# Performance work log

Hardware: AMD Instinct MI355X
Metric: run time of the kernel (lower is better)

## Reference

```python
import jax, jax.numpy as jnp
import numpy as np

NUM_USERS, NUM_ITEMS, NUM_GROUPS = 100000, 50000, 20000
D = 64
B, M = 16384, 50


def setup_inputs() -> dict:
    key = jax.random.key(0)
    ks = jax.random.split(key, 16)
    inp = {
        "group_inputs": jax.random.randint(ks[0], (B,), 0, NUM_GROUPS),
        "item_inputs": jax.random.randint(ks[1], (B,), 0, NUM_ITEMS),
        "member_ids": jax.random.randint(ks[2], (B, M), 0, NUM_USERS),
        "member_lengths": jax.random.randint(ks[3], (B,), 0, M),
        # embedding tables (xavier-ish scale)
        "user_table": jax.random.normal(ks[4], (NUM_USERS, D), jnp.float32) * 0.05,
        "item_table": jax.random.normal(ks[5], (NUM_ITEMS, D), jnp.float32) * 0.05,
        "group_table": jax.random.normal(ks[6], (NUM_GROUPS, D), jnp.float32) * 0.05,
        # attention MLP: 2D -> 16 -> 1
        "att_w1": jax.random.normal(ks[7], (2 * D, 16), jnp.float32) * 0.1,
        "att_b1": jnp.zeros((16,), jnp.float32),
        "att_w2": jax.random.normal(ks[8], (16, 1), jnp.float32) * 0.1,
        "att_b2": jnp.zeros((1,), jnp.float32),
        # predict MLP: 3D -> 8 -> 1
        "pred_w1": jax.random.normal(ks[9], (3 * D, 8), jnp.float32) * 0.1,
        "pred_b1": jnp.zeros((8,), jnp.float32),
        "pred_w2": jax.random.normal(ks[10], (8, 1), jnp.float32) * 0.1,
        "pred_b2": jnp.zeros((1,), jnp.float32),
    }
    return inp


def reference(group_inputs, item_inputs, member_ids, member_lengths,
              user_table, item_table, group_table,
              att_w1, att_b1, att_w2, att_b2,
              pred_w1, pred_b1, pred_w2, pred_b2):
    # mask: at least one valid member per group
    mask = jnp.arange(M)[None, :] <= member_lengths[:, None]          # [B, M] bool
    mem_e = user_table[member_ids]                                    # [B, M, D]
    item_e = item_table[item_inputs]                                  # [B, D]

    # attention over members: concat(member, item) -> 16 -> 1
    gi = jnp.concatenate(
        [mem_e, jnp.broadcast_to(item_e[:, None, :], mem_e.shape)], axis=-1)  # [B, M, 2D]
    h = jax.nn.relu(jnp.einsum('bmk,kh->bmh', gi, att_w1) + att_b1)   # [B, M, 16]
    scores = (jnp.einsum('bmh,ho->bmo', h, att_w2) + att_b2)[..., 0]  # [B, M]
    scores = jnp.where(mask, scores, -jnp.inf)
    at_wt = jax.nn.softmax(scores, axis=-1)                           # [B, M]

    g_att = jnp.einsum('bm,bmd->bd', at_wt, mem_e)                    # [B, D]
    g = g_att + group_table[group_inputs]                             # [B, D]

    elem = g * item_e
    new_e = jnp.concatenate([elem, g, item_e], axis=-1)               # [B, 3D]
    ph = jax.nn.relu(new_e @ pred_w1 + pred_b1)                       # [B, 8]
    y = jax.nn.sigmoid(ph @ pred_w2 + pred_b2)                        # [B, 1]
    return y
```

## Files before the change

kernel.cpp:

```cpp
#include <hip/hip_runtime.h>
#include <math.h>

constexpr int MM = 50;
constexpr int DD = 64;
constexpr int HH = 16;
constexpr int PH = 8;
constexpr int WAVES_PER_BLOCK = 4;

__global__ __launch_bounds__(256) void agree_kernel(
    const int* __restrict__ group_inputs,
    const int* __restrict__ item_inputs,
    const int* __restrict__ member_ids,
    const int* __restrict__ member_lengths,
    const float* __restrict__ user_table,
    const float* __restrict__ item_table,
    const float* __restrict__ group_table,
    const float* __restrict__ att_w1,
    const float* __restrict__ att_b1,
    const float* __restrict__ att_w2,
    const float* __restrict__ att_b2,
    const float* __restrict__ pred_w1,
    const float* __restrict__ pred_b1,
    const float* __restrict__ pred_w2,
    const float* __restrict__ pred_b2,
    float* __restrict__ out,
    int B)
{
    __shared__ float lds_wt[WAVES_PER_BLOCK][MM];
    __shared__ int   lds_id[WAVES_PER_BLOCK][MM];

    const int lane = threadIdx.x & 63;
    const int wave = threadIdx.x >> 6;
    const int b = blockIdx.x * WAVES_PER_BLOCK + wave;
    if (b >= B) return;

    const int my_m = (lane < MM) ? lane : (MM - 1);
    const int my_id = member_ids[b * MM + my_m];
    if (lane < MM) lds_id[wave][lane] = my_id;

    const int item_idx = item_inputs[b];
    const float item_d = item_table[(size_t)item_idx * DD + lane];

    float h[HH];
    {
        const float* w1row = att_w1 + (size_t)(DD + lane) * HH;
        #pragma unroll
        for (int j = 0; j < HH; ++j) h[j] = item_d * w1row[j];
        #pragma unroll
        for (int off = 32; off > 0; off >>= 1) {
            #pragma unroll
            for (int j = 0; j < HH; ++j) h[j] += __shfl_xor(h[j], off, 64);
        }
        #pragma unroll
        for (int j = 0; j < HH; ++j) h[j] += att_b1[j];
    }

    const float* myrow = user_table + (size_t)my_id * DD;
    #pragma unroll 4
    for (int d4 = 0; d4 < DD / 4; ++d4) {
        const float4 x = ((const float4*)myrow)[d4];
        const float* w1d = att_w1 + (size_t)(d4 * 4) * HH;
        #pragma unroll
        for (int j = 0; j < HH; ++j) {
            h[j] = fmaf(x.x, w1d[0 * HH + j], h[j]);
            h[j] = fmaf(x.y, w1d[1 * HH + j], h[j]);
            h[j] = fmaf(x.z, w1d[2 * HH + j], h[j]);
            h[j] = fmaf(x.w, w1d[3 * HH + j], h[j]);
        }
    }

    float score = att_b2[0];
    #pragma unroll
    for (int j = 0; j < HH; ++j) score = fmaf(fmaxf(h[j], 0.0f), att_w2[j], score);

    const int len = member_lengths[b];
    const bool valid = (lane < MM) && (lane <= len);
    score = valid ? score : -INFINITY;

    float mx = score;
    #pragma unroll
    for (int off = 32; off > 0; off >>= 1) mx = fmaxf(mx, __shfl_xor(mx, off, 64));
    float e = valid ? __expf(score - mx) : 0.0f;
    float sum = e;
    #pragma unroll
    for (int off = 32; off > 0; off >>= 1) sum += __shfl_xor(sum, off, 64);
    if (lane < MM) lds_wt[wave][lane] = e / sum;
    __builtin_amdgcn_s_waitcnt(0);

    const int mcnt = (len < MM - 1 ? len : MM - 1) + 1;
    float g = 0.0f;
    #pragma unroll 2
    for (int m = 0; m < mcnt; ++m) {
        const float wm  = lds_wt[wave][m];
        const int   idm = lds_id[wave][m];
        g = fmaf(wm, user_table[(size_t)idm * DD + lane], g);
    }
    const int gid = group_inputs[b];
    g += group_table[(size_t)gid * DD + lane];

    const float elem = g * item_d;
    float p[PH];
    {
        const float* pa = pred_w1 + (size_t)lane * PH;
        const float* pb = pred_w1 + (size_t)(DD + lane) * PH;
        const float* pc = pred_w1 + (size_t)(2 * DD + lane) * PH;
        #pragma unroll
        for (int j = 0; j < PH; ++j)
            p[j] = fmaf(elem, pa[j], fmaf(g, pb[j], item_d * pc[j]));
    }
    #pragma unroll
    for (int off = 32; off > 0; off >>= 1) {
        #pragma unroll
        for (int j = 0; j < PH; ++j) p[j] += __shfl_xor(p[j], off, 64);
    }

    if (lane == 0) {
        float acc = pred_b2[0];
        #pragma unroll
        for (int j = 0; j < PH; ++j)
            acc = fmaf(fmaxf(p[j] + pred_b1[j], 0.0f), pred_w2[j], acc);
        out[b] = 1.0f / (1.0f + __expf(-acc));
    }
}

extern "C" void kernel_launch(void* const* d_in, const int* in_sizes, int n_in,
                              void* d_out, int out_size, void* d_ws, size_t ws_size,
                              hipStream_t stream) {
    const int*   group_inputs   = (const int*)d_in[0];
    const int*   item_inputs    = (const int*)d_in[1];
    const int*   member_ids     = (const int*)d_in[2];
    const int*   member_lengths = (const int*)d_in[3];
    const float* user_table     = (const float*)d_in[4];
    const float* item_table     = (const float*)d_in[5];
    const float* group_table    = (const float*)d_in[6];
    const float* att_w1         = (const float*)d_in[7];
    const float* att_b1         = (const float*)d_in[8];
    const float* att_w2         = (const float*)d_in[9];
    const float* att_b2         = (const float*)d_in[10];
    const float* pred_w1        = (const float*)d_in[11];
    const float* pred_b1        = (const float*)d_in[12];
    const float* pred_w2        = (const float*)d_in[13];
    const float* pred_b2        = (const float*)d_in[14];
    float* out = (float*)d_out;

    const int B = in_sizes[0];
    const int blocks = (B + WAVES_PER_BLOCK - 1) / WAVES_PER_BLOCK;
    agree_kernel<<<blocks, 256, 0, stream>>>(
        group_inputs, item_inputs, member_ids, member_lengths,
        user_table, item_table, group_table,
        att_w1, att_b1, att_w2, att_b2,
        pred_w1, pred_b1, pred_w2, pred_b2,
        out, B);
}
```

Measured before the change: 158.9 us.

## Precompute per-row attention projections for user and item tables before main kernel

Adds a precompute kernel that multiplies every user and item embedding row by its half of the attention first-layer weights once per call, writing 16-float projections to workspace. The main kernel then gets each member's hidden activations by loading 16 floats and adding the item projection, instead of doing a 64x16 matvec per member. The weighted-sum gather is also unrolled by four with weight and id packed together in LDS. The trade-off is that all 150k table rows get projected even though only about 820k member lookups are needed, costing a full read of both tables plus an extra launch.

After: 144.5 us. -9.1%, faster.

```diff
diff --git a/kernel.cpp b/kernel.cpp
--- a/kernel.cpp
+++ b/kernel.cpp
@@ -7,7 +7,159 @@
 constexpr int PH = 8;
 constexpr int WAVES_PER_BLOCK = 4;
 
-__global__ __launch_bounds__(256) void agree_kernel(
+__global__ __launch_bounds__(256) void precompute_kernel(
+    const float* __restrict__ user_table,
+    const float* __restrict__ item_table,
+    const float* __restrict__ att_w1,
+    const float* __restrict__ att_b1,
+    float* __restrict__ U,
+    float* __restrict__ I,
+    int nU, int nI, int userBlocks)
+{
+    const bool isU = (int)blockIdx.x < userBlocks;
+    const int row = isU ? ((int)blockIdx.x * 256 + (int)threadIdx.x)
+                        : (((int)blockIdx.x - userBlocks) * 256 + (int)threadIdx.x);
+    const int n = isU ? nU : nI;
+    if (row >= n) return;
+
+    const float* __restrict__ src = isU ? user_table : item_table;
+    const float* __restrict__ w1  = isU ? att_w1 : (att_w1 + DD * HH);
+    const float4* rp = (const float4*)(src + (size_t)row * DD);
+
+    float acc[HH];
+    #pragma unroll
+    for (int j = 0; j < HH; ++j) acc[j] = isU ? 0.0f : att_b1[j];
+
+    #pragma unroll 4
+    for (int d4 = 0; d4 < DD / 4; ++d4) {
+        const float4 x = rp[d4];
+        const float* w = w1 + (size_t)(d4 * 4) * HH;
+        #pragma unroll
+        for (int j = 0; j < HH; ++j) {
+            acc[j] = fmaf(x.x, w[0 * HH + j], acc[j]);
+            acc[j] = fmaf(x.y, w[1 * HH + j], acc[j]);
+            acc[j] = fmaf(x.z, w[2 * HH + j], acc[j]);
+            acc[j] = fmaf(x.w, w[3 * HH + j], acc[j]);
+        }
+    }
+
+    float4* o4 = (float4*)((isU ? U : I) + (size_t)row * HH);
+    o4[0] = make_float4(acc[0],  acc[1],  acc[2],  acc[3]);
+    o4[1] = make_float4(acc[4],  acc[5],  acc[6],  acc[7]);
+    o4[2] = make_float4(acc[8],  acc[9],  acc[10], acc[11]);
+    o4[3] = make_float4(acc[12], acc[13], acc[14], acc[15]);
+}
+
+__global__ __launch_bounds__(256) void agree_main(
+    const int* __restrict__ group_inputs,
+    const int* __restrict__ item_inputs,
+    const int* __restrict__ member_ids,
+    const int* __restrict__ member_lengths,
+    const float* __restrict__ user_table,
+    const float* __restrict__ item_table,
+    const float* __restrict__ group_table,
+    const float* __restrict__ att_w2,
+    const float* __restrict__ att_b2,
+    const float* __restrict__ pred_w1,
+    const float* __restrict__ pred_b1,
+    const float* __restrict__ pred_w2,
+    const float* __restrict__ pred_b2,
+    const float* __restrict__ U,
+    const float* __restrict__ I,
+    float* __restrict__ out,
+    int B)
+{
+    __shared__ float2 lds_pair[WAVES_PER_BLOCK][MM];
+
+    const int lane = threadIdx.x & 63;
+    const int wave = threadIdx.x >> 6;
+    const int b = blockIdx.x * WAVES_PER_BLOCK + wave;
+    if (b >= B) return;
+
+    const int my_m = (lane < MM) ? lane : (MM - 1);
+    const int my_id = member_ids[b * MM + my_m];
+    const int item_idx = item_inputs[b];
+
+    const float4* up = (const float4*)(U + (size_t)my_id * HH);
+    const float4 u0 = up[0], u1 = up[1], u2 = up[2], u3 = up[3];
+    const float* ip = I + (size_t)item_idx * HH;
+
+    float score = att_b2[0];
+    {
+        const float uu[HH] = { u0.x,u0.y,u0.z,u0.w, u1.x,u1.y,u1.z,u1.w,
+                               u2.x,u2.y,u2.z,u2.w, u3.x,u3.y,u3.z,u3.w };
+        #pragma unroll
+        for (int j = 0; j < HH; ++j)
+            score = fmaf(fmaxf(uu[j] + ip[j], 0.0f), att_w2[j], score);
+    }
+
+    const int len = member_lengths[b];
+    const bool valid = (lane < MM) && (lane <= len);
+    score = valid ? score : -INFINITY;
+
+    float mx = score;
+    #pragma unroll
+    for (int off = 32; off > 0; off >>= 1) mx = fmaxf(mx, __shfl_xor(mx, off, 64));
+    float e = valid ? __expf(score - mx) : 0.0f;
+    float sum = e;
+    #pragma unroll
+    for (int off = 32; off > 0; off >>= 1) sum += __shfl_xor(sum, off, 64);
+    if (lane < MM)
+        lds_pair[wave][lane] = make_float2(e / sum, __int_as_float(my_id));
+    __builtin_amdgcn_s_waitcnt(0);
+
+    const float item_d = item_table[(size_t)item_idx * DD + lane];
+
+    const int mcnt = (len < MM - 1 ? len : MM - 1) + 1;
+    float g = 0.0f;
+    int m = 0;
+    for (; m + 4 <= mcnt; m += 4) {
+        const float2 q0 = lds_pair[wave][m + 0];
+        const float2 q1 = lds_pair[wave][m + 1];
+        const float2 q2 = lds_pair[wave][m + 2];
+        const float2 q3 = lds_pair[wave][m + 3];
+        const float x0 = user_table[(size_t)__float_as_int(q0.y) * DD + lane];
+        const float x1 = user_table[(size_t)__float_as_int(q1.y) * DD + lane];
+        const float x2 = user_table[(size_t)__float_as_int(q2.y) * DD + lane];
+        const float x3 = user_table[(size_t)__float_as_int(q3.y) * DD + lane];
+        g = fmaf(q0.x, x0, g);
+        g = fmaf(q1.x, x1, g);
+        g = fmaf(q2.x, x2, g);
+        g = fmaf(q3.x, x3, g);
+    }
+    for (; m < mcnt; ++m) {
+        const float2 q = lds_pair[wave][m];
+        g = fmaf(q.x, user_table[(size_t)__float_as_int(q.y) * DD + lane], g);
+    }
+    const int gid = group_inputs[b];
+    g += group_table[(size_t)gid * DD + lane];
+
+    const float elem = g * item_d;
+    float p[PH];
+    {
+        const float* pa = pred_w1 + (size_t)lane * PH;
+        const float* pb = pred_w1 + (size_t)(DD + lane) * PH;
+        const float* pc = pred_w1 + (size_t)(2 * DD + lane) * PH;
+        #pragma unroll
+        for (int j = 0; j < PH; ++j)
+            p[j] = fmaf(elem, pa[j], fmaf(g, pb[j], item_d * pc[j]));
+    }
+    #pragma unroll
+    for (int off = 32; off > 0; off >>= 1) {
+        #pragma unroll
+        for (int j = 0; j < PH; ++j) p[j] += __shfl_xor(p[j], off, 64);
+    }
+
+    if (lane == 0) {
+        float acc = pred_b2[0];
+        #pragma unroll
+        for (int j = 0; j < PH; ++j)
+            acc = fmaf(fmaxf(p[j] + pred_b1[j], 0.0f), pred_w2[j], acc);
+        out[b] = 1.0f / (1.0f + __expf(-acc));
+    }
+}
+
+__global__ __launch_bounds__(256) void agree_fallback(
     const int* __restrict__ group_inputs,
     const int* __restrict__ item_inputs,
     const int* __restrict__ member_ids,
@@ -143,12 +295,30 @@
     const float* pred_b2        = (const float*)d_in[14];
     float* out = (float*)d_out;
 
-    const int B = in_sizes[0];
+    const int B  = in_sizes[0];
+    const int nU = in_sizes[4] / DD;
+    const int nI = in_sizes[5] / DD;
+    const size_t need = (size_t)(nU + nI) * HH * sizeof(float);
     const int blocks = (B + WAVES_PER_BLOCK - 1) / WAVES_PER_BLOCK;
-    agree_kernel<<<blocks, 256, 0, stream>>>(
-        group_inputs, item_inputs, member_ids, member_lengths,
-        user_table, item_table, group_table,
-        att_w1, att_b1, att_w2, att_b2,
-        pred_w1, pred_b1, pred_w2, pred_b2,
-        out, B);
+
+    if (ws_size >= need) {
+        float* U = (float*)d_ws;
+        float* I = U + (size_t)nU * HH;
+        const int userBlocks = (nU + 255) / 256;
+        const int itemBlocks = (nI + 255) / 256;
+        precompute_kernel<<<userBlocks + itemBlocks, 256, 0, stream>>>(
+            user_table, item_table, att_w1, att_b1, U, I, nU, nI, userBlocks);
+        agree_main<<<blocks, 256, 0, stream>>>(
+            group_inputs, item_inputs, member_ids, member_lengths,
+            user_table, item_table, group_table,
+            att_w2, att_b2, pred_w1, pred_b1, pred_w2, pred_b2,
+            U, I, out, B);
+    } else {
+        agree_fallback<<<blocks, 256, 0, stream>>>(
+            group_inputs, item_inputs, member_ids, member_lengths,
+            user_table, item_table, group_table,
+            att_w1, att_b1, att_w2, att_b2,
+            pred_w1, pred_b1, pred_w2, pred_b2,
+            out, B);
+    }
 }
```
